# Performance work log

Measured on AMD Instinct MI355X. Metric: run time of the kernel, lower is better.

## Reference

```python
import jax, jax.numpy as jnp
import numpy as np

N_NODES = 100000
N_EDGES = 3200000
IN_FEATS = 512
HIDDEN = 16
OUT_FEATS = 128
N_CLASSES = 3


def _glorot(key, shape):
    fan_in, fan_out = shape[0], shape[1]
    limit = float(np.sqrt(6.0 / (fan_in + fan_out)))
    return jax.random.uniform(key, shape, jnp.float32, -limit, limit)


def setup_inputs() -> dict:
    key = jax.random.key(0)
    ks = jax.random.split(key, 9)
    features = jax.random.normal(ks[0], (N_NODES, IN_FEATS), jnp.float32)
    src = jax.random.randint(ks[1], (N_EDGES,), 0, N_NODES, jnp.int64)
    dst = jax.random.randint(ks[2], (N_EDGES,), 0, N_NODES, jnp.int64)
    W1 = _glorot(ks[3], (IN_FEATS, HIDDEN))
    b1 = jnp.zeros((HIDDEN,), jnp.float32)
    W2 = _glorot(ks[4], (HIDDEN, OUT_FEATS))
    b2 = jnp.zeros((OUT_FEATS,), jnp.float32)
    lim = float(1.0 / np.sqrt(OUT_FEATS))
    Wfc = jax.random.uniform(ks[5], (OUT_FEATS, N_CLASSES), jnp.float32, -lim, lim)
    bfc = jax.random.uniform(ks[6], (N_CLASSES,), jnp.float32, -lim, lim)
    return {"features": features, "src": src, "dst": dst,
            "W1": W1, "b1": b1, "W2": W2, "b2": b2, "Wfc": Wfc, "bfc": bfc}


def _graph_conv(feat, src, dst, W, b):
    # DGL GraphConv, norm='both': D_out^{-1/2} A D_in^{-1/2} feat W + b
    ones = jnp.ones((src.shape[0],), feat.dtype)
    deg_out = jax.ops.segment_sum(ones, src, num_segments=N_NODES)
    deg_in = jax.ops.segment_sum(ones, dst, num_segments=N_NODES)
    norm_src = jax.lax.rsqrt(jnp.maximum(deg_out, 1.0))  # [N]
    norm_dst = jax.lax.rsqrt(jnp.maximum(deg_in, 1.0))   # [N]
    # project first (in >= out here), then aggregate over edges
    h = (feat * norm_src[:, None]) @ W                   # [N, out]
    agg = jax.ops.segment_sum(h[src], dst, num_segments=N_NODES)  # [N, out]
    return agg * norm_dst[:, None] + b


def reference(features, src, dst, W1, b1, W2, b2, Wfc, bfc):
    x = jax.nn.relu(_graph_conv(features, src, dst, W1, b1))
    x = _graph_conv(x, src, dst, W2, b2)
    return x @ Wfc + bfc
```

## Files before the change

kernel.cpp:

```cpp
#include <hip/hip_runtime.h>

#define N_NODES 100000
#define N_EDGES 3200000
#define F_IN 512
#define NH 16
#define F_OUT 128
#define NCLS 3

#define NB 782
#define BCAP 4736
#define CHUNK 4096

typedef float  f32x4 __attribute__((ext_vector_type(4)));
typedef short  s16x8 __attribute__((ext_vector_type(8)));

static __device__ __forceinline__ short f2bf(float f) {
    union { float f; unsigned u; } v; v.f = f;
    unsigned r = v.u + 0x7FFFu + ((v.u >> 16) & 1u);
    return (short)(r >> 16);
}

__global__ __launch_bounds__(256) void bin_scatter_kernel(const int* __restrict__ src,
                                                          const int* __restrict__ dst,
                                                          int* __restrict__ deg_out,
                                                          int* __restrict__ gcursor,
                                                          int* __restrict__ pairbuf) {
    __shared__ int hist[NB];
    __shared__ int base[NB];
    int t = threadIdx.x;
    for (int i = t; i < NB; i += 256) hist[i] = 0;
    __syncthreads();
    int e0 = blockIdx.x * CHUNK;
    int nE = N_EDGES - e0; if (nE > CHUNK) nE = CHUNK;
    int pk[16], bk[16], rk[16];
#pragma unroll
    for (int it = 0; it < 16; ++it) {
        int i = t + it * 256;
        bool valid = i < nE;
        int s = valid ? src[e0 + i] : 0;
        int d = valid ? dst[e0 + i] : 0;
        if (valid) atomicAdd(&deg_out[s], 1);
        int b = d >> 7;
        pk[it] = s | ((d & 127) << 17);
        bk[it] = b;
        rk[it] = valid ? atomicAdd(&hist[b], 1) : 0;
    }
    __syncthreads();
    int rot = blockIdx.x % NB;
    for (int j = t; j < NB; j += 256) {
        int b = j + rot; if (b >= NB) b -= NB;
        int h = hist[b];
        base[b] = (h > 0) ? atomicAdd(&gcursor[b], h) : 0;
    }
    __syncthreads();
#pragma unroll
    for (int it = 0; it < 16; ++it) {
        int i = t + it * 256;
        if (i < nE) {
            int b = bk[it];
            int pos = base[b] + rk[it];
            if (pos < BCAP) pairbuf[b * BCAP + pos] = pk[it];
        }
    }
}

__global__ __launch_bounds__(1024) void bucket_scan_kernel(const int* __restrict__ gcursor,
                                                           int* __restrict__ csr_base) {
    __shared__ int s[1024];
    int t = threadIdx.x;
    int v = 0;
    if (t < NB) { v = gcursor[t]; if (v > BCAP) v = BCAP; }
    s[t] = v;
    __syncthreads();
    for (int off = 1; off < 1024; off <<= 1) {
        int x = (t >= off) ? s[t - off] : 0;
        __syncthreads();
        s[t] += x;
        __syncthreads();
    }
    if (t < NB) csr_base[t] = s[t] - v;
}

__global__ __launch_bounds__(256) void bucket_csr_kernel(const int* __restrict__ gcursor,
                                                         const int* __restrict__ csr_base,
                                                         const int* __restrict__ pairbuf,
                                                         int* __restrict__ col,
                                                         int* __restrict__ row_ptr,
                                                         float* __restrict__ norm_dst) {
    __shared__ int hist[128];
    __shared__ int scn[128];
    int b = blockIdx.x;
    int t = threadIdx.x;
    if (t < 128) hist[t] = 0;
    __syncthreads();
    int c = gcursor[b]; if (c > BCAP) c = BCAP;
    const int* pb = pairbuf + b * BCAP;
    int pk[19], rk[19];
#pragma unroll
    for (int it = 0; it < 19; ++it) {
        int i = t + it * 256;
        bool valid = i < c;
        int v = valid ? pb[i] : 0;
        pk[it] = v;
        rk[it] = valid ? atomicAdd(&hist[v >> 17], 1) : 0;
    }
    __syncthreads();
    if (t < 128) scn[t] = hist[t];
    __syncthreads();
    for (int off = 1; off < 128; off <<= 1) {
        int x = (t >= off && t < 128) ? scn[t - off] : 0;
        __syncthreads();
        if (t < 128) scn[t] += x;
        __syncthreads();
    }
    int gbase = csr_base[b];
#pragma unroll
    for (int it = 0; it < 19; ++it) {
        int i = t + it * 256;
        if (i < c) {
            int v = pk[it];
            int node = v >> 17;
            int pos = gbase + (scn[node] - hist[node]) + rk[it];
            col[pos] = v & 0x1FFFF;
        }
    }
    int node = b * 128 + t;
    if (t < 128 && node < N_NODES) {
        row_ptr[node] = gbase + scn[t] - hist[t];
        norm_dst[node] = rsqrtf(fmaxf((float)hist[t], 1.0f));
    }
    if (b == NB - 1 && t == 0) row_ptr[N_NODES] = N_EDGES;
}

__global__ void norm_src_kernel(const int* __restrict__ deg_out, float* __restrict__ norm_src) {
    int i = blockIdx.x * blockDim.x + threadIdx.x;
    if (i < N_NODES) norm_src[i] = rsqrtf(fmaxf((float)deg_out[i], 1.0f));
}

__global__ void w1b_prep_kernel(const float* __restrict__ W1, unsigned short* __restrict__ W1B) {
    int idx = blockIdx.x * blockDim.x + threadIdx.x;
    if (idx >= 16 * 64 * 8) return;
    int kc = idx >> 9, lane = (idx >> 3) & 63, i = idx & 7;
    int k = kc * 32 + (lane >> 4) * 8 + i;
    int j = lane & 15;
    W1B[idx] = (unsigned short)f2bf(W1[k * NH + j]);
}

__global__ void wc_prep_kernel(const float* __restrict__ W2, const float* __restrict__ b2,
                               const float* __restrict__ Wfc, const float* __restrict__ bfc,
                               float* __restrict__ Wc) {
    int t = threadIdx.x;
    if (t < NH * NCLS) {
        int j = t / NCLS, c = t % NCLS;
        float acc = 0.0f;
        for (int k = 0; k < F_OUT; ++k) acc += W2[j * F_OUT + k] * Wfc[k * NCLS + c];
        Wc[t] = acc;
    } else if (t < NH * NCLS + NCLS) {
        int c = t - NH * NCLS;
        float acc = bfc[c];
        for (int k = 0; k < F_OUT; ++k) acc += b2[k] * Wfc[k * NCLS + c];
        Wc[t] = acc;
    }
}

__global__ __launch_bounds__(256) void gemm1_kernel(const float* __restrict__ feat,
                                                    const unsigned short* __restrict__ W1B,
                                                    const float* __restrict__ norm_src,
                                                    float* __restrict__ h1) {
    int t = threadIdx.x;
    int lane = t & 63;
    int m = lane & 15;
    int q = lane >> 4;
    const s16x8* wb = (const s16x8*)W1B;
    s16x8 B[16];
#pragma unroll
    for (int kc = 0; kc < 16; ++kc) B[kc] = wb[kc * 64 + lane];

    int w = blockIdx.x * 4 + (t >> 6);
    int nwaves = gridDim.x * 4;
    const int ntiles = N_NODES / 16;
    for (int tile = w; tile < ntiles; tile += nwaves) {
        f32x4 acc = {0.0f, 0.0f, 0.0f, 0.0f};
        const float* arow = feat + (size_t)(tile * 16 + m) * F_IN + q * 8;
#pragma unroll
        for (int kc = 0; kc < 16; ++kc) {
            f32x4 fa = *(const f32x4*)(arow + kc * 32);
            f32x4 fb = *(const f32x4*)(arow + kc * 32 + 4);
            s16x8 a;
            a[0] = f2bf(fa.x); a[1] = f2bf(fa.y); a[2] = f2bf(fa.z); a[3] = f2bf(fa.w);
            a[4] = f2bf(fb.x); a[5] = f2bf(fb.y); a[6] = f2bf(fb.z); a[7] = f2bf(fb.w);
            acc = __builtin_amdgcn_mfma_f32_16x16x32_bf16(a, B[kc], acc, 0, 0, 0);
        }
#pragma unroll
        for (int r = 0; r < 4; ++r) {
            int node = tile * 16 + q * 4 + r;
            h1[(size_t)node * NH + m] = acc[r] * norm_src[node];
        }
    }
}

__global__ __launch_bounds__(256) void agg1_kernel(const int* __restrict__ row_ptr,
                                                   const int* __restrict__ col,
                                                   const float* __restrict__ h1,
                                                   const float* __restrict__ norm_dst,
                                                   const float* __restrict__ norm_src,
                                                   const float* __restrict__ b1,
                                                   float* __restrict__ x1n) {
    int t = threadIdx.x;
    int lane = t & 63;
    int n = blockIdx.x * 4 + (t >> 6);
    int eo = lane >> 2, comp = lane & 3;
    int beg = row_ptr[n], end = row_ptr[n + 1];
    f32x4 acc = {0.0f, 0.0f, 0.0f, 0.0f};
    for (int e = beg + eo; e < end; e += 16) {
        int s = col[e];
        acc += *(const f32x4*)(h1 + (size_t)s * NH + comp * 4);
    }
#pragma unroll
    for (int sh = 4; sh <= 32; sh <<= 1) {
        acc.x += __shfl_xor(acc.x, sh); acc.y += __shfl_xor(acc.y, sh);
        acc.z += __shfl_xor(acc.z, sh); acc.w += __shfl_xor(acc.w, sh);
    }
    if (lane < 4) {
        float nd = norm_dst[n], ns = norm_src[n];
        f32x4 bv = ((const f32x4*)b1)[lane];
        f32x4 v = acc * nd + bv;
        v.x = fmaxf(v.x, 0.0f) * ns; v.y = fmaxf(v.y, 0.0f) * ns;
        v.z = fmaxf(v.z, 0.0f) * ns; v.w = fmaxf(v.w, 0.0f) * ns;
        ((f32x4*)(x1n + (size_t)n * NH))[lane] = v;
    }
}

__global__ __launch_bounds__(256) void agg2_kernel(const int* __restrict__ row_ptr,
                                                   const int* __restrict__ col,
                                                   const float* __restrict__ x1n,
                                                   const float* __restrict__ norm_dst,
                                                   const float* __restrict__ Wc,
                                                   float* __restrict__ out) {
    __shared__ float Wcs[NH * NCLS + NCLS];
    int t = threadIdx.x;
    if (t < NH * NCLS + NCLS) Wcs[t] = Wc[t];
    __syncthreads();
    int lane = t & 63;
    int n = blockIdx.x * 4 + (t >> 6);
    int eo = lane >> 2, comp = lane & 3;
    int beg = row_ptr[n], end = row_ptr[n + 1];
    f32x4 acc = {0.0f, 0.0f, 0.0f, 0.0f};
    for (int e = beg + eo; e < end; e += 16) {
        int s = col[e];
        acc += *(const f32x4*)(x1n + (size_t)s * NH + comp * 4);
    }
#pragma unroll
    for (int sh = 4; sh <= 32; sh <<= 1) {
        acc.x += __shfl_xor(acc.x, sh); acc.y += __shfl_xor(acc.y, sh);
        acc.z += __shfl_xor(acc.z, sh); acc.w += __shfl_xor(acc.w, sh);
    }
    float p0 = 0.0f, p1 = 0.0f, p2 = 0.0f;
    if (lane < 4) {
#pragma unroll
        for (int i = 0; i < 4; ++i) {
            float y = acc[i];
            int j = lane * 4 + i;
            p0 += y * Wcs[j * NCLS + 0];
            p1 += y * Wcs[j * NCLS + 1];
            p2 += y * Wcs[j * NCLS + 2];
        }
    }
    p0 += __shfl_xor(p0, 1); p0 += __shfl_xor(p0, 2);
    p1 += __shfl_xor(p1, 1); p1 += __shfl_xor(p1, 2);
    p2 += __shfl_xor(p2, 1); p2 += __shfl_xor(p2, 2);
    if (lane == 0) {
        float nd = norm_dst[n];
        out[(size_t)n * NCLS + 0] = nd * p0 + Wcs[NH * NCLS + 0];
        out[(size_t)n * NCLS + 1] = nd * p1 + Wcs[NH * NCLS + 1];
        out[(size_t)n * NCLS + 2] = nd * p2 + Wcs[NH * NCLS + 2];
    }
}

extern "C" void kernel_launch(void* const* d_in, const int* in_sizes, int n_in,
                              void* d_out, int out_size, void* d_ws, size_t ws_size,
                              hipStream_t stream) {
    const float* feat = (const float*)d_in[0];
    const int*   src  = (const int*)d_in[1];
    const int*   dst  = (const int*)d_in[2];
    const float* W1   = (const float*)d_in[3];
    const float* b1   = (const float*)d_in[4];
    const float* W2   = (const float*)d_in[5];
    const float* b2   = (const float*)d_in[6];
    const float* Wfc  = (const float*)d_in[7];
    const float* bfc  = (const float*)d_in[8];
    float* out = (float*)d_out;

    char* ws = (char*)d_ws;
    size_t off = 0;
    auto carve = [&](size_t bytes) {
        char* p = ws + off;
        off = (off + bytes + 255) & ~(size_t)255;
        return p;
    };
    int*   deg_out  = (int*)carve((size_t)N_NODES * 4);
    int*   gcursor  = (int*)carve((size_t)NB * 4);
    int*   csr_base = (int*)carve((size_t)NB * 4);
    int*   pairbuf  = (int*)carve((size_t)NB * BCAP * 4);
    int*   row_ptr  = (int*)carve((size_t)(N_NODES + 1) * 4);
    int*   col      = (int*)carve((size_t)N_EDGES * 4);
    float* norm_src = (float*)carve((size_t)N_NODES * 4);
    float* norm_dst = (float*)carve((size_t)N_NODES * 4);
    float* h1       = (float*)carve((size_t)N_NODES * NH * 4);
    float* x1n      = (float*)carve((size_t)N_NODES * NH * 4);
    unsigned short* W1B = (unsigned short*)carve(16 * 64 * 8 * 2);
    float* Wc       = (float*)carve((NH * NCLS + NCLS) * 4);
    (void)ws_size;

    hipMemsetAsync(deg_out, 0, (size_t)N_NODES * 4, stream);
    hipMemsetAsync(gcursor, 0, (size_t)NB * 4, stream);

    const int nBinBlocks = (N_EDGES + CHUNK - 1) / CHUNK;
    bin_scatter_kernel<<<nBinBlocks, 256, 0, stream>>>(src, dst, deg_out, gcursor, pairbuf);
    bucket_scan_kernel<<<1, 1024, 0, stream>>>(gcursor, csr_base);
    bucket_csr_kernel<<<NB, 256, 0, stream>>>(gcursor, csr_base, pairbuf, col, row_ptr, norm_dst);

    norm_src_kernel<<<(N_NODES + 255) / 256, 256, 0, stream>>>(deg_out, norm_src);

    w1b_prep_kernel<<<32, 256, 0, stream>>>(W1, W1B);
    wc_prep_kernel<<<1, 64, 0, stream>>>(W2, b2, Wfc, bfc, Wc);

    gemm1_kernel<<<625, 256, 0, stream>>>(feat, W1B, norm_src, h1);

    agg1_kernel<<<N_NODES / 4, 256, 0, stream>>>(row_ptr, col, h1, norm_dst, norm_src, b1, x1n);

    agg2_kernel<<<N_NODES / 4, 256, 0, stream>>>(row_ptr, col, x1n, norm_dst, Wc, out);
}
```

Baseline: 599.8 us.

## Store intermediates in bf16, rework binning pass, fold norm_src into consumers

Hidden features h1 and x1n are now stored as bf16 instead of fp32, which halves the bytes gathered per edge in both aggregation kernels. The binning kernel now makes two passes over src/dst with larger chunks and 512 threads, and ranks items with shared-memory atomics on a cursor instead of keeping them in registers. The norm_src kernel and its buffer are removed, and rsqrt of deg_out is computed inline where it is used. gemm1's grid is doubled. Storing intermediates in bf16 adds rounding error, and the re-read of edges adds global traffic in the binning step.

Measured after the change: 592.9 us. No clear change (-1.1%).

```diff
diff --git a/kernel.cpp b/kernel.cpp
--- a/kernel.cpp
+++ b/kernel.cpp
@@ -9,58 +9,54 @@
 
 #define NB 782
 #define BCAP 4736
-#define CHUNK 4096
+#define CHUNK 16384
 
 typedef float  f32x4 __attribute__((ext_vector_type(4)));
 typedef short  s16x8 __attribute__((ext_vector_type(8)));
-
-static __device__ __forceinline__ short f2bf(float f) {
+typedef unsigned short u16x4 __attribute__((ext_vector_type(4)));
+
+static __device__ __forceinline__ unsigned short f2bf(float f) {
     union { float f; unsigned u; } v; v.f = f;
     unsigned r = v.u + 0x7FFFu + ((v.u >> 16) & 1u);
-    return (short)(r >> 16);
-}
-
-__global__ __launch_bounds__(256) void bin_scatter_kernel(const int* __restrict__ src,
-                                                          const int* __restrict__ dst,
-                                                          int* __restrict__ deg_out,
-                                                          int* __restrict__ gcursor,
-                                                          int* __restrict__ pairbuf) {
+    return (unsigned short)(r >> 16);
+}
+static __device__ __forceinline__ float bf2f(unsigned short u) {
+    union { unsigned u; float f; } v; v.u = ((unsigned)u) << 16;
+    return v.f;
+}
+
+__global__ __launch_bounds__(512) void bin_kernel(const int* __restrict__ src,
+                                                  const int* __restrict__ dst,
+                                                  int* __restrict__ deg_out,
+                                                  int* __restrict__ gcursor,
+                                                  int* __restrict__ pairbuf) {
     __shared__ int hist[NB];
-    __shared__ int base[NB];
-    int t = threadIdx.x;
-    for (int i = t; i < NB; i += 256) hist[i] = 0;
+    __shared__ int cur[NB];
+    int t = threadIdx.x;
+    for (int i = t; i < NB; i += 512) hist[i] = 0;
     __syncthreads();
     int e0 = blockIdx.x * CHUNK;
     int nE = N_EDGES - e0; if (nE > CHUNK) nE = CHUNK;
-    int pk[16], bk[16], rk[16];
-#pragma unroll
-    for (int it = 0; it < 16; ++it) {
-        int i = t + it * 256;
-        bool valid = i < nE;
-        int s = valid ? src[e0 + i] : 0;
-        int d = valid ? dst[e0 + i] : 0;
-        if (valid) atomicAdd(&deg_out[s], 1);
-        int b = d >> 7;
-        pk[it] = s | ((d & 127) << 17);
-        bk[it] = b;
-        rk[it] = valid ? atomicAdd(&hist[b], 1) : 0;
+    for (int i = t; i < nE; i += 512) {
+        int s = src[e0 + i];
+        int d = dst[e0 + i];
+        atomicAdd(&deg_out[s], 1);
+        atomicAdd(&hist[d >> 7], 1);
     }
     __syncthreads();
     int rot = blockIdx.x % NB;
-    for (int j = t; j < NB; j += 256) {
+    for (int j = t; j < NB; j += 512) {
         int b = j + rot; if (b >= NB) b -= NB;
         int h = hist[b];
-        base[b] = (h > 0) ? atomicAdd(&gcursor[b], h) : 0;
-    }
-    __syncthreads();
-#pragma unroll
-    for (int it = 0; it < 16; ++it) {
-        int i = t + it * 256;
-        if (i < nE) {
-            int b = bk[it];
-            int pos = base[b] + rk[it];
-            if (pos < BCAP) pairbuf[b * BCAP + pos] = pk[it];
-        }
+        cur[b] = (h > 0) ? atomicAdd(&gcursor[b], h) : 0;
+    }
+    __syncthreads();
+    for (int i = t; i < nE; i += 512) {
+        int s = src[e0 + i];
+        int d = dst[e0 + i];
+        int b = d >> 7;
+        int pos = atomicAdd(&cur[b], 1);
+        if (pos < BCAP) pairbuf[b * BCAP + pos] = s | ((d & 127) << 17);
     }
 }
 
@@ -94,7 +90,7 @@
     if (t < 128) hist[t] = 0;
     __syncthreads();
     int c = gcursor[b]; if (c > BCAP) c = BCAP;
-    const int* pb = pairbuf + b * BCAP;
+    const int* pb = pairbuf + (size_t)b * BCAP;
     int pk[19], rk[19];
 #pragma unroll
     for (int it = 0; it < 19; ++it) {
@@ -132,18 +128,13 @@
     if (b == NB - 1 && t == 0) row_ptr[N_NODES] = N_EDGES;
 }
 
-__global__ void norm_src_kernel(const int* __restrict__ deg_out, float* __restrict__ norm_src) {
-    int i = blockIdx.x * blockDim.x + threadIdx.x;
-    if (i < N_NODES) norm_src[i] = rsqrtf(fmaxf((float)deg_out[i], 1.0f));
-}
-
 __global__ void w1b_prep_kernel(const float* __restrict__ W1, unsigned short* __restrict__ W1B) {
     int idx = blockIdx.x * blockDim.x + threadIdx.x;
     if (idx >= 16 * 64 * 8) return;
     int kc = idx >> 9, lane = (idx >> 3) & 63, i = idx & 7;
     int k = kc * 32 + (lane >> 4) * 8 + i;
     int j = lane & 15;
-    W1B[idx] = (unsigned short)f2bf(W1[k * NH + j]);
+    W1B[idx] = f2bf(W1[k * NH + j]);
 }
 
 __global__ void wc_prep_kernel(const float* __restrict__ W2, const float* __restrict__ b2,
@@ -165,8 +156,8 @@
 
 __global__ __launch_bounds__(256) void gemm1_kernel(const float* __restrict__ feat,
                                                     const unsigned short* __restrict__ W1B,
-                                                    const float* __restrict__ norm_src,
-                                                    float* __restrict__ h1) {
+                                                    const int* __restrict__ deg_out,
+                                                    unsigned short* __restrict__ h1b) {
     int t = threadIdx.x;
     int lane = t & 63;
     int m = lane & 15;
@@ -194,18 +185,19 @@
 #pragma unroll
         for (int r = 0; r < 4; ++r) {
             int node = tile * 16 + q * 4 + r;
-            h1[(size_t)node * NH + m] = acc[r] * norm_src[node];
+            float ns = rsqrtf(fmaxf((float)deg_out[node], 1.0f));
+            h1b[(size_t)node * NH + m] = f2bf(acc[r] * ns);
         }
     }
 }
 
 __global__ __launch_bounds__(256) void agg1_kernel(const int* __restrict__ row_ptr,
                                                    const int* __restrict__ col,
-                                                   const float* __restrict__ h1,
+                                                   const unsigned short* __restrict__ h1b,
                                                    const float* __restrict__ norm_dst,
-                                                   const float* __restrict__ norm_src,
+                                                   const int* __restrict__ deg_out,
                                                    const float* __restrict__ b1,
-                                                   float* __restrict__ x1n) {
+                                                   unsigned short* __restrict__ x1nb) {
     int t = threadIdx.x;
     int lane = t & 63;
     int n = blockIdx.x * 4 + (t >> 6);
@@ -214,7 +206,9 @@
     f32x4 acc = {0.0f, 0.0f, 0.0f, 0.0f};
     for (int e = beg + eo; e < end; e += 16) {
         int s = col[e];
-        acc += *(const f32x4*)(h1 + (size_t)s * NH + comp * 4);
+        u16x4 hv = *(const u16x4*)(h1b + (size_t)s * NH + comp * 4);
+        acc.x += bf2f(hv.x); acc.y += bf2f(hv.y);
+        acc.z += bf2f(hv.z); acc.w += bf2f(hv.w);
     }
 #pragma unroll
     for (int sh = 4; sh <= 32; sh <<= 1) {
@@ -222,18 +216,20 @@
         acc.z += __shfl_xor(acc.z, sh); acc.w += __shfl_xor(acc.w, sh);
     }
     if (lane < 4) {
-        float nd = norm_dst[n], ns = norm_src[n];
+        float nd = norm_dst[n];
+        float ns = rsqrtf(fmaxf((float)deg_out[n], 1.0f));
         f32x4 bv = ((const f32x4*)b1)[lane];
         f32x4 v = acc * nd + bv;
-        v.x = fmaxf(v.x, 0.0f) * ns; v.y = fmaxf(v.y, 0.0f) * ns;
-        v.z = fmaxf(v.z, 0.0f) * ns; v.w = fmaxf(v.w, 0.0f) * ns;
-        ((f32x4*)(x1n + (size_t)n * NH))[lane] = v;
+        u16x4 o;
+        o.x = f2bf(fmaxf(v.x, 0.0f) * ns); o.y = f2bf(fmaxf(v.y, 0.0f) * ns);
+        o.z = f2bf(fmaxf(v.z, 0.0f) * ns); o.w = f2bf(fmaxf(v.w, 0.0f) * ns);
+        *(u16x4*)(x1nb + (size_t)n * NH + lane * 4) = o;
     }
 }
 
 __global__ __launch_bounds__(256) void agg2_kernel(const int* __restrict__ row_ptr,
                                                    const int* __restrict__ col,
-                                                   const float* __restrict__ x1n,
+                                                   const unsigned short* __restrict__ x1nb,
                                                    const float* __restrict__ norm_dst,
                                                    const float* __restrict__ Wc,
                                                    float* __restrict__ out) {
@@ -248,7 +244,9 @@
     f32x4 acc = {0.0f, 0.0f, 0.0f, 0.0f};
     for (int e = beg + eo; e < end; e += 16) {
         int s = col[e];
-        acc += *(const f32x4*)(x1n + (size_t)s * NH + comp * 4);
+        u16x4 hv = *(const u16x4*)(x1nb + (size_t)s * NH + comp * 4);
+        acc.x += bf2f(hv.x); acc.y += bf2f(hv.y);
+        acc.z += bf2f(hv.z); acc.w += bf2f(hv.w);
     }
 #pragma unroll
     for (int sh = 4; sh <= 32; sh <<= 1) {
@@ -304,11 +302,10 @@
     int*   pairbuf  = (int*)carve((size_t)NB * BCAP * 4);
     int*   row_ptr  = (int*)carve((size_t)(N_NODES + 1) * 4);
     int*   col      = (int*)carve((size_t)N_EDGES * 4);
-    float* norm_src = (float*)carve((size_t)N_NODES * 4);
     float* norm_dst = (float*)carve((size_t)N_NODES * 4);
-    float* h1       = (float*)carve((size_t)N_NODES * NH * 4);
-    float* x1n      = (float*)carve((size_t)N_NODES * NH * 4);
-    unsigned short* W1B = (unsigned short*)carve(16 * 64 * 8 * 2);
+    unsigned short* h1b  = (unsigned short*)carve((size_t)N_NODES * NH * 2);
+    unsigned short* x1nb = (unsigned short*)carve((size_t)N_NODES * NH * 2);
+    unsigned short* W1B  = (unsigned short*)carve(16 * 64 * 8 * 2);
     float* Wc       = (float*)carve((NH * NCLS + NCLS) * 4);
     (void)ws_size;
 
@@ -316,18 +313,16 @@
     hipMemsetAsync(gcursor, 0, (size_t)NB * 4, stream);
 
     const int nBinBlocks = (N_EDGES + CHUNK - 1) / CHUNK;
-    bin_scatter_kernel<<<nBinBlocks, 256, 0, stream>>>(src, dst, deg_out, gcursor, pairbuf);
+    bin_kernel<<<nBinBlocks, 512, 0, stream>>>(src, dst, deg_out, gcursor, pairbuf);
     bucket_scan_kernel<<<1, 1024, 0, stream>>>(gcursor, csr_base);
     bucket_csr_kernel<<<NB, 256, 0, stream>>>(gcursor, csr_base, pairbuf, col, row_ptr, norm_dst);
 
-    norm_src_kernel<<<(N_NODES + 255) / 256, 256, 0, stream>>>(deg_out, norm_src);
-
     w1b_prep_kernel<<<32, 256, 0, stream>>>(W1, W1B);
     wc_prep_kernel<<<1, 64, 0, stream>>>(W2, b2, Wfc, bfc, Wc);
 
-    gemm1_kernel<<<625, 256, 0, stream>>>(feat, W1B, norm_src, h1);
-
-    agg1_kernel<<<N_NODES / 4, 256, 0, stream>>>(row_ptr, col, h1, norm_dst, norm_src, b1, x1n);
-
-    agg2_kernel<<<N_NODES / 4, 256, 0, stream>>>(row_ptr, col, x1n, norm_dst, Wc, out);
-}
+    gemm1_kernel<<<1250, 256, 0, stream>>>(feat, W1B, deg_out, h1b);
+
+    agg1_kernel<<<N_NODES / 4, 256, 0, stream>>>(row_ptr, col, h1b, norm_dst, deg_out, b1, x1nb);
+
+    agg2_kernel<<<N_NODES / 4, 256, 0, stream>>>(row_ptr, col, x1nb, norm_dst, Wc, out);
+}
```
